# Kernel tuning notes

Measured on AMD Instinct MI355X. Metric: run time of the kernel, lower is better.

Reference implementation:

```python
import jax, jax.numpy as jnp
import numpy as np

# Dimensions (match init_kwargs)
B, N, D = 128, 256, 256   # batch, n_agents, obs_dim
MSG = 64                  # msg_dim
CD = 32                   # compressed_dim = int(msg_dim * 0.5)
K = 8                     # top-k recipients
H1, H2 = 128, 256         # msg_gen hidden, receiver hidden


def setup_inputs() -> dict:
    key = jax.random.key(0)
    ks = jax.random.split(key, 16)
    s = 0.02
    # All weights stored (in_features, out_features): y = x @ W + b
    return {
        "obs_all": jax.random.normal(ks[0], (B, N, D), dtype=jnp.float32),
        "W1": jax.random.normal(ks[1], (D, H1), dtype=jnp.float32) * s,
        "b1": jnp.zeros((H1,), jnp.float32),
        "W2": jax.random.normal(ks[2], (H1, MSG), dtype=jnp.float32) * s,
        "b2": jnp.zeros((MSG,), jnp.float32),
        "Wc": jax.random.normal(ks[3], (MSG, CD), dtype=jnp.float32) * s,
        "bc": jnp.zeros((CD,), jnp.float32),
        "Wd": jax.random.normal(ks[4], (CD, MSG), dtype=jnp.float32) * s,
        "bd": jnp.zeros((MSG,), jnp.float32),
        "Wbil": jax.random.normal(ks[5], (D, D), dtype=jnp.float32) * s,  # Bilinear weight (out=1)
        "bbil": jnp.zeros((), jnp.float32),
        "Wr1": jax.random.normal(ks[6], (D + MSG, H2), dtype=jnp.float32) * s,
        "br1": jnp.zeros((H2,), jnp.float32),
        "Wr2": jax.random.normal(ks[7], (H2, D), dtype=jnp.float32) * s,
        "br2": jnp.zeros((D,), jnp.float32),
    }


def reference(obs_all, W1, b1, W2, b2, Wc, bc, Wd, bd, Wbil, bbil, Wr1, br1, Wr2, br2):
    # send: msg_gen MLP -> compress -> decompress (all agents at once)
    h = jax.nn.relu(jnp.einsum('bnd,dh->bnh', obs_all, W1) + b1)
    full_msg = jnp.einsum('bnh,hm->bnm', h, W2) + b2          # (B, N, MSG)
    compressed = jnp.einsum('bnm,mc->bnc', full_msg, Wc) + bc  # (B, N, CD)
    msgs = jnp.einsum('bnc,cm->bnm', compressed, Wd) + bd      # (B, N, MSG)

    # pairwise bilinear relevance: scores[b,i,j] = obs_i^T Wbil obs_j + bias
    tmp = jnp.einsum('bid,de->bie', obs_all, Wbil)
    scores = jnp.einsum('bie,bje->bij', tmp, obs_all) + bbil   # (B, N, N)

    # top-k gating: softmax over the k selected scores, zeros elsewhere
    topk_vals, topk_idx = jax.lax.top_k(scores, K)             # (B, N, K)
    gate_vals = jax.nn.softmax(topk_vals, axis=-1)             # (B, N, K)

    # weighted aggregation of selected messages (honor top-k sparsity:
    # gather the K messages per receiver instead of building dense gates)
    sel_msgs = jax.vmap(lambda m, ix: m[ix])(msgs, topk_idx)   # (B, N, K, MSG)
    agg = jnp.einsum('bik,bikm->bim', gate_vals, sel_msgs)     # (B, N, MSG)

    # receive: MLP over [obs, aggregated message]
    combined = jnp.concatenate([obs_all, agg], axis=-1)        # (B, N, D+MSG)
    r = jax.nn.relu(jnp.einsum('bnc,ch->bnh', combined, Wr1) + br1)
    enriched = jnp.einsum('bnh,hd->bnd', r, Wr2) + br2          # (B, N, D)
    return enriched
```

## Files before the change

### kernel.cpp

```cpp
#include <hip/hip_runtime.h>
#include <cstddef>

#define BB   128
#define NN   256
#define DIMD 256
#define MSG  64
#define CDIM 32
#define TOPK 8
#define H1D  128
#define H2D  256
#define BN   (BB*NN)

typedef unsigned short u16;
typedef u16   u16x4  __attribute__((ext_vector_type(4)));
typedef u16   u16x8  __attribute__((ext_vector_type(8)));
typedef short short8 __attribute__((ext_vector_type(8)));
typedef float f32x4  __attribute__((ext_vector_type(4)));

__device__ __forceinline__ u16 f2bf(float f) {
    return (u16)((__float_as_uint(f) + 0x8000u) >> 16);
}
__device__ __forceinline__ float bf2f(u16 u) {
    return __uint_as_float(((unsigned)u) << 16);
}
__device__ __forceinline__ u16 bf2key(u16 b) {
    return (u16)(b ^ ((b & 0x8000u) ? 0xFFFFu : 0x8000u));
}
__device__ __forceinline__ u16 key2bf(u16 k) {
    return (u16)(k ^ ((k & 0x8000u) ? 0x8000u : 0xFFFFu));
}
#define MFMA16(a,b,c) __builtin_amdgcn_mfma_f32_16x16x32_bf16((a),(b),(c),0,0,0)


__global__ __launch_bounds__(256) void prep_w_k(
    const float* __restrict__ W1, const float* __restrict__ W2,
    const float* __restrict__ Wc, const float* __restrict__ Wd,
    const float* __restrict__ Wb, const float* __restrict__ Wr1,
    const float* __restrict__ Wr2,
    u16* __restrict__ Wp1, u16* __restrict__ Wp2, u16* __restrict__ Wpc,
    u16* __restrict__ Wpd, u16* __restrict__ WpB, u16* __restrict__ Wpr1,
    u16* __restrict__ Wpr2)
{
    const int t = blockIdx.x * 256 + threadIdx.x;
    const float* src; u16* dst; int I, os, loc;
    if      (t <  32768) { src = W1;  dst = Wp1;  I = 256; os = 7; loc = t; }
    else if (t <  40960) { src = W2;  dst = Wp2;  I = 128; os = 6; loc = t - 32768; }
    else if (t <  43008) { src = Wc;  dst = Wpc;  I = 64;  os = 5; loc = t - 40960; }
    else if (t <  45056) { src = Wd;  dst = Wpd;  I = 32;  os = 6; loc = t - 43008; }
    else if (t < 110592) { src = Wb;  dst = WpB;  I = 256; os = 8; loc = t - 45056; }
    else if (t < 192512) { src = Wr1; dst = Wpr1; I = 320; os = 8; loc = t - 110592; }
    else                 { src = Wr2; dst = Wpr2; I = 256; os = 8; loc = t - 192512; }
    const int i = loc >> os;
    const int o = loc & ((1 << os) - 1);
    const int nt = o >> 4, ls = o & 15;
    const int KB = I >> 5;
    const int kk = i >> 5, q = (i & 31) >> 3, j = i & 7;
    dst[((size_t)(nt*KB + kk)*64 + q*16 + ls)*8 + j] = f2bf(src[loc]);
}

__global__ __launch_bounds__(256) __attribute__((amdgpu_waves_per_eu(4, 4)))
void sendpack_k(
    const float* __restrict__ obs, u16* __restrict__ obs_p,
    const u16* __restrict__ Wp1, const float* __restrict__ b1,
    const u16* __restrict__ Wp2, const float* __restrict__ b2,
    const u16* __restrict__ Wpc, const float* __restrict__ bc,
    const u16* __restrict__ Wpd, const float* __restrict__ bd,
    u16* __restrict__ msgs_bf)
{
    __shared__ __align__(16) u16 sO[32][264];
    __shared__ __align__(16) u16 sH[32][136];
    __shared__ __align__(16) u16 sF[32][72];
    __shared__ __align__(16) u16 sC[32][40];
    const int t = threadIdx.x;
    const int w = t >> 6, l = t & 63, q = l >> 4, ls = l & 15;
    const int row0 = blockIdx.x * 32;
    const int tile0 = blockIdx.x * 2;

    {
        const float4* src = (const float4*)(obs + (size_t)row0 * 256);
        #pragma unroll
        for (int i = 0; i < 8; ++i) {
            const int idx = t + 256*i;
            const int r = idx >> 6, c4 = idx & 63;
            const float4 v = src[idx];
            u16x4 o;
            o[0] = f2bf(v.x); o[1] = f2bf(v.y); o[2] = f2bf(v.z); o[3] = f2bf(v.w);
            *(u16x4*)&sO[r][c4*4] = o;
        }
    }
    __syncthreads();
    {
        #pragma unroll
        for (int i = 0; i < 4; ++i) {
            const int u = t + 256*i;
            const int tile = u >> 9, kk = (u >> 6) & 7, lane = u & 63;
            const u16x8 v = *(const u16x8*)&sO[tile*16 + (lane & 15)][kk*32 + (lane >> 4)*8];
            *(u16x8*)(obs_p + (size_t)(tile0 + tile)*4096 + (size_t)(kk*64 + lane)*8) = v;
        }
    }
    {
        f32x4 acc[2][2];
        #pragma unroll
        for (int mi = 0; mi < 2; ++mi)
            #pragma unroll
            for (int nn = 0; nn < 2; ++nn) acc[mi][nn] = (f32x4){0,0,0,0};
        short8 cb[2];
        #pragma unroll
        for (int nn = 0; nn < 2; ++nn)
            cb[nn] = *(const short8*)(Wp1 + ((size_t)((w*2+nn)*8))*512 + l*8);
        #pragma unroll
        for (int kk = 0; kk < 8; ++kk) {
            short8 nb[2];
            if (kk < 7) {
                #pragma unroll
                for (int nn = 0; nn < 2; ++nn)
                    nb[nn] = *(const short8*)(Wp1 + ((size_t)((w*2+nn)*8 + kk+1))*512 + l*8);
            }
            short8 a[2];
            a[0] = *(const short8*)&sO[ls][kk*32 + q*8];
            a[1] = *(const short8*)&sO[16 + ls][kk*32 + q*8];
            #pragma unroll
            for (int mi = 0; mi < 2; ++mi)
                #pragma unroll
                for (int nn = 0; nn < 2; ++nn)
                    acc[mi][nn] = MFMA16(a[mi], cb[nn], acc[mi][nn]);
            if (kk < 7) {
                #pragma unroll
                for (int nn = 0; nn < 2; ++nn) cb[nn] = nb[nn];
            }
        }
        #pragma unroll
        for (int nn = 0; nn < 2; ++nn) {
            const float bv = b1[(w*2+nn)*16 + ls];
            #pragma unroll
            for (int mi = 0; mi < 2; ++mi)
                #pragma unroll
                for (int r = 0; r < 4; ++r)
                    sH[mi*16 + q*4 + r][(w*2+nn)*16 + ls] = f2bf(fmaxf(acc[mi][nn][r] + bv, 0.0f));
        }
    }
    __syncthreads();
    {
        f32x4 acc[2];
        acc[0] = (f32x4){0,0,0,0}; acc[1] = (f32x4){0,0,0,0};
        #pragma unroll
        for (int kk = 0; kk < 4; ++kk) {
            const int k0 = kk * 32;
            short8 a[2];
            a[0] = *(const short8*)(&sH[ls][k0 + q*8]);
            a[1] = *(const short8*)(&sH[16 + ls][k0 + q*8]);
            const short8 bf = *(const short8*)(Wp2 + ((size_t)(w*4 + kk)*64 + l)*8);
            acc[0] = MFMA16(a[0], bf, acc[0]);
            acc[1] = MFMA16(a[1], bf, acc[1]);
        }
        const float bv = b2[w*16 + ls];
        #pragma unroll
        for (int mi = 0; mi < 2; ++mi)
            #pragma unroll
            for (int r = 0; r < 4; ++r)
                sF[mi*16 + q*4 + r][w*16 + ls] = f2bf(acc[mi][r] + bv);
    }
    __syncthreads();
    if (w < 2) {
        f32x4 acc[2];
        acc[0] = (f32x4){0,0,0,0}; acc[1] = (f32x4){0,0,0,0};
        #pragma unroll
        for (int kk = 0; kk < 2; ++kk) {
            const int k0 = kk * 32;
            short8 a[2];
            a[0] = *(const short8*)(&sF[ls][k0 + q*8]);
            a[1] = *(const short8*)(&sF[16 + ls][k0 + q*8]);
            const short8 bf = *(const short8*)(Wpc + ((size_t)(w*2 + kk)*64 + l)*8);
            acc[0] = MFMA16(a[0], bf, acc[0]);
            acc[1] = MFMA16(a[1], bf, acc[1]);
        }
        const float bv = bc[w*16 + ls];
        #pragma unroll
        for (int mi = 0; mi < 2; ++mi)
            #pragma unroll
            for (int r = 0; r < 4; ++r)
                sC[mi*16 + q*4 + r][w*16 + ls] = f2bf(acc[mi][r] + bv);
    }
    __syncthreads();
    {
        f32x4 acc[2];
        acc[0] = (f32x4){0,0,0,0}; acc[1] = (f32x4){0,0,0,0};
        short8 a[2];
        a[0] = *(const short8*)(&sC[ls][q*8]);
        a[1] = *(const short8*)(&sC[16 + ls][q*8]);
        const short8 bf = *(const short8*)(Wpd + ((size_t)w*64 + l)*8);
        acc[0] = MFMA16(a[0], bf, acc[0]);
        acc[1] = MFMA16(a[1], bf, acc[1]);
        const float bv = bd[w*16 + ls];
        #pragma unroll
        for (int mi = 0; mi < 2; ++mi)
            #pragma unroll
            for (int r = 0; r < 4; ++r)
                msgs_bf[(size_t)(row0 + mi*16 + q*4 + r)*MSG + w*16 + ls] = f2bf(acc[mi][r] + bv);
    }
}

__global__ __launch_bounds__(512) __attribute__((amdgpu_waves_per_eu(4, 4)))
void relrecv_k(
    const u16* __restrict__ obs_p, const u16* __restrict__ WpB,
    const float* __restrict__ bbil, const u16* __restrict__ msgs_bf,
    const u16* __restrict__ Wpr1, const float* __restrict__ br1,
    const u16* __restrict__ Wpr2, const float* __restrict__ br2,
    float* __restrict__ out)
{
    __shared__ __align__(16) u16 sS[64][264];
    __shared__ __align__(16) u16 sA[64][72];
    __shared__ __align__(16) u16 sObs[16384];
    __shared__ float sG[64][8];
    __shared__ __align__(16) unsigned short sI[64][8];
    const int t = threadIdx.x;
    const int w = t >> 6, l = t & 63, q = l >> 4, ls = l & 15;
    const int bid = blockIdx.x;
    const int xcd = bid & 7, idx = bid >> 3;
    const int b   = xcd * 16 + (idx >> 2);
    const int mc  = idx & 3;
    const int row0g = b * NN + mc * 64;
    const int mt0   = b * 16 + mc * 4;

    short8 pb[4][2];

    {
        const u16x8* src = (const u16x8*)(obs_p + (size_t)mt0 * 4096);
        #pragma unroll
        for (int i = 0; i < 4; ++i)
            *(u16x8*)&sObs[(t + 512*i) * 8] = src[t + 512*i];
    }
    #pragma unroll
    for (int d = 0; d < 3; ++d)
        #pragma unroll
        for (int nn = 0; nn < 2; ++nn)
            pb[d][nn] = *(const short8*)(WpB + ((size_t)((w*2+nn)*8 + d))*512 + l*8);
    __syncthreads();

    {
        f32x4 acc[4][2];
        #pragma unroll
        for (int mi = 0; mi < 4; ++mi)
            #pragma unroll
            for (int nn = 0; nn < 2; ++nn) acc[mi][nn] = (f32x4){0,0,0,0};
        #pragma unroll
        for (int kk = 0; kk < 8; ++kk) {
            if (kk < 5) {
                #pragma unroll
                for (int nn = 0; nn < 2; ++nn)
                    pb[(kk+3)&3][nn] = *(const short8*)(WpB + ((size_t)((w*2+nn)*8 + kk+3))*512 + l*8);
            }
            short8 a[4];
            #pragma unroll
            for (int mi = 0; mi < 4; ++mi)
                a[mi] = *(const short8*)&sObs[mi*4096 + kk*512 + l*8];
            #pragma unroll
            for (int mi = 0; mi < 4; ++mi)
                #pragma unroll
                for (int nn = 0; nn < 2; ++nn)
                    acc[mi][nn] = MFMA16(a[mi], pb[kk&3][nn], acc[mi][nn]);
        }
        #pragma unroll
        for (int mi = 0; mi < 4; ++mi)
            #pragma unroll
            for (int nn = 0; nn < 2; ++nn)
                #pragma unroll
                for (int r = 0; r < 4; ++r)
                    sS[mi*16 + q*4 + r][(w*2+nn)*16 + ls] = f2bf(acc[mi][nn][r]);
    }
    #pragma unroll
    for (int d = 0; d < 3; ++d)
        #pragma unroll
        for (int nn = 0; nn < 2; ++nn)
            pb[d][nn] = *(const short8*)(obs_p + ((size_t)((b*16 + w*2+nn)*8 + d))*512 + l*8);
    __syncthreads();

    {
        const float bb = bbil[0];
        f32x4 acc[4][2];
        #pragma unroll
        for (int mi = 0; mi < 4; ++mi)
            #pragma unroll
            for (int nn = 0; nn < 2; ++nn) acc[mi][nn] = (f32x4){0,0,0,0};
        #pragma unroll
        for (int kk = 0; kk < 8; ++kk) {
            if (kk < 5) {
                #pragma unroll
                for (int nn = 0; nn < 2; ++nn)
                    pb[(kk+3)&3][nn] = *(const short8*)(obs_p + ((size_t)((b*16 + w*2+nn)*8 + kk+3))*512 + l*8);
            }
            const int k0 = kk * 32;
            short8 a[4];
            #pragma unroll
            for (int mi = 0; mi < 4; ++mi)
                a[mi] = *(const short8*)(&sS[mi*16 + ls][k0 + q*8]);
            #pragma unroll
            for (int mi = 0; mi < 4; ++mi)
                #pragma unroll
                for (int nn = 0; nn < 2; ++nn)
                    acc[mi][nn] = MFMA16(a[mi], pb[kk&3][nn], acc[mi][nn]);
        }
        __syncthreads();
        #pragma unroll
        for (int mi = 0; mi < 4; ++mi)
            #pragma unroll
            for (int nn = 0; nn < 2; ++nn)
                #pragma unroll
                for (int r = 0; r < 4; ++r)
                    sS[mi*16 + q*4 + r][(w*2+nn)*16 + ls] = bf2key(f2bf(acc[mi][nn][r] + bb));
    }
    __syncthreads();
    {
        const int r = t >> 3, g = t & 7;
        u16 buf[32];
        #pragma unroll
        for (int c = 0; c < 4; ++c)
            *(u16x8*)&buf[c*8] = *(const u16x8*)&sS[r][g*32 + c*8];
        unsigned val[8];
        #pragma unroll
        for (int j = 0; j < 8; ++j) val[j] = 0u;
        #pragma unroll
        for (int i = 0; i < 32; ++i) {
            const unsigned p = ((unsigned)buf[i] << 8) | (unsigned)(255 - (g*32 + i));
            if (p > val[7]) {
                #pragma unroll
                for (int j = 7; j >= 1; --j) {
                    const bool cj  = p > val[j];
                    const bool cjm = p > val[j-1];
                    val[j] = cj ? (cjm ? val[j-1] : p) : val[j];
                }
                val[0] = p > val[0] ? p : val[0];
            }
        }
        unsigned wv[8];
        #pragma unroll
        for (int k = 0; k < 8; ++k) {
            unsigned h = val[0], o;
            o = (unsigned)__shfl_xor((int)h, 1); h = o > h ? o : h;
            o = (unsigned)__shfl_xor((int)h, 2); h = o > h ? o : h;
            o = (unsigned)__shfl_xor((int)h, 4); h = o > h ? o : h;
            wv[k] = h;
            const bool won = (val[0] == h);
            #pragma unroll
            for (int j = 0; j < 7; ++j) val[j] = won ? val[j+1] : val[j];
            val[7] = won ? 0u : val[7];
        }
        if (g == 0) {
            float v[8];
            #pragma unroll
            for (int k = 0; k < 8; ++k)
                v[k] = bf2f(key2bf((u16)(wv[k] >> 8)));
            float e[8]; float s = 0.0f;
            #pragma unroll
            for (int k = 0; k < 8; ++k) { e[k] = __expf(v[k] - v[0]); s += e[k]; }
            const float inv = 1.0f / s;
            #pragma unroll
            for (int k = 0; k < 8; ++k) {
                sG[r][k] = e[k] * inv;
                sI[r][k] = (unsigned short)(255 - (wv[k] & 255u));
            }
        }
    }
    #pragma unroll
    for (int d = 0; d < 3; ++d)
        #pragma unroll
        for (int nn = 0; nn < 2; ++nn)
            pb[d][nn] = *(const short8*)(Wpr1 + ((size_t)((w*2+nn)*10 + d))*512 + l*8);
    {
        const u16* mb = msgs_bf + (size_t)b*NN*MSG + l;
        #pragma unroll
        for (int rb = 0; rb < 2; ++rb) {
            const int r0 = w*8 + rb*4;
            u16x8 id[4];
            #pragma unroll
            for (int rr = 0; rr < 4; ++rr)
                id[rr] = *(const u16x8*)&sI[r0 + rr][0];
            u16 mv[4][8];
            #pragma unroll
            for (int rr = 0; rr < 4; ++rr)
                #pragma unroll
                for (int k = 0; k < 8; ++k)
                    mv[rr][k] = mb[(size_t)id[rr][k]*MSG];
            #pragma unroll
            for (int rr = 0; rr < 4; ++rr) {
                float a = 0.0f;
                #pragma unroll
                for (int k = 0; k < 8; ++k)
                    a = fmaf(sG[r0 + rr][k], bf2f(mv[rr][k]), a);
                sA[r0 + rr][l] = f2bf(a);
            }
        }
    }
    __syncthreads();
    {
        f32x4 acc[4][2];
        #pragma unroll
        for (int mi = 0; mi < 4; ++mi)
            #pragma unroll
            for (int nn = 0; nn < 2; ++nn) acc[mi][nn] = (f32x4){0,0,0,0};
        #pragma unroll
        for (int kk = 0; kk < 10; ++kk) {
            if (kk < 7) {
                #pragma unroll
                for (int nn = 0; nn < 2; ++nn)
                    pb[(kk+3)&3][nn] = *(const short8*)(Wpr1 + ((size_t)((w*2+nn)*10 + kk+3))*512 + l*8);
            }
            short8 a[4];
            if (kk < 8) {
                #pragma unroll
                for (int mi = 0; mi < 4; ++mi)
                    a[mi] = *(const short8*)&sObs[mi*4096 + kk*512 + l*8];
            } else {
                #pragma unroll
                for (int mi = 0; mi < 4; ++mi)
                    a[mi] = *(const short8*)&sA[mi*16 + ls][(kk-8)*32 + q*8];
            }
            #pragma unroll
            for (int mi = 0; mi < 4; ++mi)
                #pragma unroll
                for (int nn = 0; nn < 2; ++nn)
                    acc[mi][nn] = MFMA16(a[mi], pb[kk&3][nn], acc[mi][nn]);
        }
        #pragma unroll
        for (int d = 0; d < 3; ++d)
            #pragma unroll
            for (int nn = 0; nn < 2; ++nn)
                pb[d][nn] = *(const short8*)(Wpr2 + ((size_t)((w*2+nn)*8 + d))*512 + l*8);
        __syncthreads();
        #pragma unroll
        for (int nn = 0; nn < 2; ++nn) {
            const float bv = br1[(w*2+nn)*16 + ls];
            #pragma unroll
            for (int mi = 0; mi < 4; ++mi)
                #pragma unroll
                for (int r = 0; r < 4; ++r)
                    sS[mi*16 + q*4 + r][(w*2+nn)*16 + ls] = f2bf(fmaxf(acc[mi][nn][r] + bv, 0.0f));
        }
    }
    __syncthreads();
    {
        f32x4 acc[4][2];
        #pragma unroll
        for (int mi = 0; mi < 4; ++mi)
            #pragma unroll
            for (int nn = 0; nn < 2; ++nn) acc[mi][nn] = (f32x4){0,0,0,0};
        #pragma unroll
        for (int kk = 0; kk < 8; ++kk) {
            if (kk < 5) {
                #pragma unroll
                for (int nn = 0; nn < 2; ++nn)
                    pb[(kk+3)&3][nn] = *(const short8*)(Wpr2 + ((size_t)((w*2+nn)*8 + kk+3))*512 + l*8);
            }
            const int k0 = kk * 32;
            short8 a[4];
            #pragma unroll
            for (int mi = 0; mi < 4; ++mi)
                a[mi] = *(const short8*)(&sS[mi*16 + ls][k0 + q*8]);
            #pragma unroll
            for (int mi = 0; mi < 4; ++mi)
                #pragma unroll
                for (int nn = 0; nn < 2; ++nn)
                    acc[mi][nn] = MFMA16(a[mi], pb[kk&3][nn], acc[mi][nn]);
        }
        #pragma unroll
        for (int nn = 0; nn < 2; ++nn) {
            const float bv = br2[(w*2+nn)*16 + ls];
            #pragma unroll
            for (int mi = 0; mi < 4; ++mi)
                #pragma unroll
                for (int r = 0; r < 4; ++r)
                    out[(size_t)(row0g + mi*16 + q*4 + r)*DIMD + (w*2+nn)*16 + ls] = acc[mi][nn][r] + bv;
        }
    }
}

extern "C" void kernel_launch(void* const* d_in, const int* in_sizes, int n_in,
                              void* d_out, int out_size, void* d_ws, size_t ws_size,
                              hipStream_t stream)
{
    (void)in_sizes; (void)n_in; (void)out_size; (void)ws_size;
    const float* obs  = (const float*)d_in[0];
    const float* W1   = (const float*)d_in[1];
    const float* b1   = (const float*)d_in[2];
    const float* W2   = (const float*)d_in[3];
    const float* b2   = (const float*)d_in[4];
    const float* Wc   = (const float*)d_in[5];
    const float* bc   = (const float*)d_in[6];
    const float* Wd   = (const float*)d_in[7];
    const float* bd   = (const float*)d_in[8];
    const float* Wbil = (const float*)d_in[9];
    const float* bbil = (const float*)d_in[10];
    const float* Wr1  = (const float*)d_in[11];
    const float* br1  = (const float*)d_in[12];
    const float* Wr2  = (const float*)d_in[13];
    const float* br2  = (const float*)d_in[14];
    float* outp = (float*)d_out;

    u16* obs_p   = (u16*)d_ws;
    u16* msgs_bf = obs_p   + (size_t)BN*256;
    u16* Wp1  = msgs_bf + (size_t)BN*64;
    u16* Wp2  = Wp1  + 32768;
    u16* Wpc  = Wp2  + 8192;
    u16* Wpd  = Wpc  + 2048;
    u16* WpB  = Wpd  + 2048;
    u16* Wpr1 = WpB  + 65536;
    u16* Wpr2 = Wpr1 + 81920;

    prep_w_k<<<1008, 256, 0, stream>>>(W1, W2, Wc, Wd, Wbil, Wr1, Wr2,
                                       Wp1, Wp2, Wpc, Wpd, WpB, Wpr1, Wpr2);
    sendpack_k<<<BN/32, 256, 0, stream>>>(obs, obs_p, Wp1, b1, Wp2, b2,
                                          Wpc, bc, Wpd, bd, msgs_bf);
    relrecv_k<<<BN/64, 512, 0, stream>>>(obs_p, WpB, bbil, msgs_bf,
                                         Wpr1, br1, Wpr2, br2, outp);
}
```

Measured before the change: 56.56 us.

## Drop shared obs staging, shrink B-fragment prefetch ring, raise waves-per-EU target

Removes the 32 KB shared-memory copy of the block's obs tile and reads obs A-fragments directly from global memory, twice (bilinear first GEMM and receiver first GEMM). The B-fragment prefetch ring drops from four stages, three ahead, to two-stage double buffering, and the waves-per-EU hint goes from exactly 4 to a minimum of 6. The aim is to cut LDS and register pressure so more blocks fit per CU and hide latency. The cost is shallower prefetch and repeated global/L2 reads of obs inside the MFMA loops.

```diff
diff --git a/kernel.cpp b/kernel.cpp
--- a/kernel.cpp
+++ b/kernel.cpp
@@ -200,7 +200,7 @@
     }
 }
 
-__global__ __launch_bounds__(512) __attribute__((amdgpu_waves_per_eu(4, 4)))
+__global__ __launch_bounds__(512) __attribute__((amdgpu_waves_per_eu(6)))
 void relrecv_k(
     const u16* __restrict__ obs_p, const u16* __restrict__ WpB,
     const float* __restrict__ bbil, const u16* __restrict__ msgs_bf,
@@ -210,7 +210,6 @@
 {
     __shared__ __align__(16) u16 sS[64][264];
     __shared__ __align__(16) u16 sA[64][72];
-    __shared__ __align__(16) u16 sObs[16384];
     __shared__ float sG[64][8];
     __shared__ __align__(16) unsigned short sI[64][8];
     const int t = threadIdx.x;
@@ -222,20 +221,11 @@
     const int row0g = b * NN + mc * 64;
     const int mt0   = b * 16 + mc * 4;
 
-    short8 pb[4][2];
-
-    {
-        const u16x8* src = (const u16x8*)(obs_p + (size_t)mt0 * 4096);
-        #pragma unroll
-        for (int i = 0; i < 4; ++i)
-            *(u16x8*)&sObs[(t + 512*i) * 8] = src[t + 512*i];
-    }
+    short8 pb[2][2];
+
     #pragma unroll
-    for (int d = 0; d < 3; ++d)
-        #pragma unroll
-        for (int nn = 0; nn < 2; ++nn)
-            pb[d][nn] = *(const short8*)(WpB + ((size_t)((w*2+nn)*8 + d))*512 + l*8);
-    __syncthreads();
+    for (int nn = 0; nn < 2; ++nn)
+        pb[0][nn] = *(const short8*)(WpB + ((size_t)((w*2+nn)*8))*512 + l*8);
 
     {
         f32x4 acc[4][2];
@@ -245,20 +235,21 @@
             for (int nn = 0; nn < 2; ++nn) acc[mi][nn] = (f32x4){0,0,0,0};
         #pragma unroll
         for (int kk = 0; kk < 8; ++kk) {
-            if (kk < 5) {
-                #pragma unroll
-                for (int nn = 0; nn < 2; ++nn)
-                    pb[(kk+3)&3][nn] = *(const short8*)(WpB + ((size_t)((w*2+nn)*8 + kk+3))*512 + l*8);
+            const int cur = kk & 1, nxt = cur ^ 1;
+            if (kk < 7) {
+                #pragma unroll
+                for (int nn = 0; nn < 2; ++nn)
+                    pb[nxt][nn] = *(const short8*)(WpB + ((size_t)((w*2+nn)*8 + kk+1))*512 + l*8);
             }
             short8 a[4];
             #pragma unroll
             for (int mi = 0; mi < 4; ++mi)
-                a[mi] = *(const short8*)&sObs[mi*4096 + kk*512 + l*8];
-            #pragma unroll
-            for (int mi = 0; mi < 4; ++mi)
-                #pragma unroll
-                for (int nn = 0; nn < 2; ++nn)
-                    acc[mi][nn] = MFMA16(a[mi], pb[kk&3][nn], acc[mi][nn]);
+                a[mi] = *(const short8*)(obs_p + ((size_t)((mt0+mi)*8 + kk))*512 + l*8);
+            #pragma unroll
+            for (int mi = 0; mi < 4; ++mi)
+                #pragma unroll
+                for (int nn = 0; nn < 2; ++nn)
+                    acc[mi][nn] = MFMA16(a[mi], pb[cur][nn], acc[mi][nn]);
         }
         #pragma unroll
         for (int mi = 0; mi < 4; ++mi)
@@ -269,10 +260,8 @@
                     sS[mi*16 + q*4 + r][(w*2+nn)*16 + ls] = f2bf(acc[mi][nn][r]);
     }
     #pragma unroll
-    for (int d = 0; d < 3; ++d)
-        #pragma unroll
-        for (int nn = 0; nn < 2; ++nn)
-            pb[d][nn] = *(const short8*)(obs_p + ((size_t)((b*16 + w*2+nn)*8 + d))*512 + l*8);
+    for (int nn = 0; nn < 2; ++nn)
+        pb[0][nn] = *(const short8*)(obs_p + ((size_t)((b*16 + w*2+nn)*8))*512 + l*8);
     __syncthreads();
 
     {
@@ -284,10 +273,11 @@
             for (int nn = 0; nn < 2; ++nn) acc[mi][nn] = (f32x4){0,0,0,0};
         #pragma unroll
         for (int kk = 0; kk < 8; ++kk) {
-            if (kk < 5) {
-                #pragma unroll
-                for (int nn = 0; nn < 2; ++nn)
-                    pb[(kk+3)&3][nn] = *(const short8*)(obs_p + ((size_t)((b*16 + w*2+nn)*8 + kk+3))*512 + l*8);
+            const int cur = kk & 1, nxt = cur ^ 1;
+            if (kk < 7) {
+                #pragma unroll
+                for (int nn = 0; nn < 2; ++nn)
+                    pb[nxt][nn] = *(const short8*)(obs_p + ((size_t)((b*16 + w*2+nn)*8 + kk+1))*512 + l*8);
             }
             const int k0 = kk * 32;
             short8 a[4];
@@ -298,7 +288,7 @@
             for (int mi = 0; mi < 4; ++mi)
                 #pragma unroll
                 for (int nn = 0; nn < 2; ++nn)
-                    acc[mi][nn] = MFMA16(a[mi], pb[kk&3][nn], acc[mi][nn]);
+                    acc[mi][nn] = MFMA16(a[mi], pb[cur][nn], acc[mi][nn]);
         }
         __syncthreads();
         #pragma unroll
@@ -362,10 +352,8 @@
         }
     }
     #pragma unroll
-    for (int d = 0; d < 3; ++d)
-        #pragma unroll
-        for (int nn = 0; nn < 2; ++nn)
-            pb[d][nn] = *(const short8*)(Wpr1 + ((size_t)((w*2+nn)*10 + d))*512 + l*8);
+    for (int nn = 0; nn < 2; ++nn)
+        pb[0][nn] = *(const short8*)(Wpr1 + ((size_t)((w*2+nn)*10))*512 + l*8);
     {
         const u16* mb = msgs_bf + (size_t)b*NN*MSG + l;
         #pragma unroll
@@ -400,16 +388,17 @@
             for (int nn = 0; nn < 2; ++nn) acc[mi][nn] = (f32x4){0,0,0,0};
         #pragma unroll
         for (int kk = 0; kk < 10; ++kk) {
-            if (kk < 7) {
-                #pragma unroll
-                for (int nn = 0; nn < 2; ++nn)
-                    pb[(kk+3)&3][nn] = *(const short8*)(Wpr1 + ((size_t)((w*2+nn)*10 + kk+3))*512 + l*8);
+            const int cur = kk & 1, nxt = cur ^ 1;
+            if (kk < 9) {
+                #pragma unroll
+                for (int nn = 0; nn < 2; ++nn)
+                    pb[nxt][nn] = *(const short8*)(Wpr1 + ((size_t)((w*2+nn)*10 + kk+1))*512 + l*8);
             }
             short8 a[4];
             if (kk < 8) {
                 #pragma unroll
                 for (int mi = 0; mi < 4; ++mi)
-                    a[mi] = *(const short8*)&sObs[mi*4096 + kk*512 + l*8];
+                    a[mi] = *(const short8*)(obs_p + ((size_t)((mt0+mi)*8 + kk))*512 + l*8);
             } else {
                 #pragma unroll
                 for (int mi = 0; mi < 4; ++mi)
@@ -419,13 +408,11 @@
             for (int mi = 0; mi < 4; ++mi)
                 #pragma unroll
                 for (int nn = 0; nn < 2; ++nn)
-                    acc[mi][nn] = MFMA16(a[mi], pb[kk&3][nn], acc[mi][nn]);
-        }
-        #pragma unroll
-        for (int d = 0; d < 3; ++d)
-            #pragma unroll
-            for (int nn = 0; nn < 2; ++nn)
-                pb[d][nn] = *(const short8*)(Wpr2 + ((size_t)((w*2+nn)*8 + d))*512 + l*8);
+                    acc[mi][nn] = MFMA16(a[mi], pb[cur][nn], acc[mi][nn]);
+        }
+        #pragma unroll
+        for (int nn = 0; nn < 2; ++nn)
+            pb[0][nn] = *(const short8*)(Wpr2 + ((size_t)((w*2+nn)*8))*512 + l*8);
         __syncthreads();
         #pragma unroll
         for (int nn = 0; nn < 2; ++nn) {
@@ -446,10 +433,11 @@
             for (int nn = 0; nn < 2; ++nn) acc[mi][nn] = (f32x4){0,0,0,0};
         #pragma unroll
         for (int kk = 0; kk < 8; ++kk) {
-            if (kk < 5) {
-                #pragma unroll
-                for (int nn = 0; nn < 2; ++nn)
-                    pb[(kk+3)&3][nn] = *(const short8*)(Wpr2 + ((size_t)((w*2+nn)*8 + kk+3))*512 + l*8);
+            const int cur = kk & 1, nxt = cur ^ 1;
+            if (kk < 7) {
+                #pragma unroll
+                for (int nn = 0; nn < 2; ++nn)
+                    pb[nxt][nn] = *(const short8*)(Wpr2 + ((size_t)((w*2+nn)*8 + kk+1))*512 + l*8);
             }
             const int k0 = kk * 32;
             short8 a[4];
@@ -460,7 +448,7 @@
             for (int mi = 0; mi < 4; ++mi)
                 #pragma unroll
                 for (int nn = 0; nn < 2; ++nn)
-                    acc[mi][nn] = MFMA16(a[mi], pb[kk&3][nn], acc[mi][nn]);
+                    acc[mi][nn] = MFMA16(a[mi], pb[cur][nn], acc[mi][nn]);
         }
         #pragma unroll
         for (int nn = 0; nn < 2; ++nn) {
```

Result: slower. 77.94 us (+37.8%).
